# Kernel tuning notes

Hardware: AMD Instinct MI355X
Metric: run time of the kernel (lower is better)

The kernel has to match this reference:

```python
import jax, jax.numpy as jnp
import numpy as np

PARENTS = np.array([0, 0, 1, 2, 3, 0, 5, 6, 7, 0, 9, 10, 11, 12, 11, 14, 15, 16, 11, 18, 19, 20])
SPARSE_JOINTS = [0, 4, 8, 13, 17, 21]
EE = np.array(SPARSE_JOINTS[1:])                       # end effectors (skip root)
NO_SPARSE = np.array([i for i in range(22) if i not in SPARSE_JOINTS])
LAMBDA_EE = 1.0
LAMBDA_EE_REG = 0.1
IDENT_DQ = np.array([1, 0, 0, 0, 0, 0, 0, 0], dtype=np.float32)


def qmul(a, b):
    # Hamilton product, (w, x, y, z) convention
    aw, ax, ay, az = a[..., 0], a[..., 1], a[..., 2], a[..., 3]
    bw, bx, by, bz = b[..., 0], b[..., 1], b[..., 2], b[..., 3]
    return jnp.stack([
        aw * bw - ax * bx - ay * by - az * bz,
        aw * bx + ax * bw + ay * bz - az * by,
        aw * by - ax * bz + ay * bw + az * bx,
        aw * bz + ax * by - ay * bx + az * bw,
    ], axis=-1)


def qconj(q):
    return q * jnp.array([1.0, -1.0, -1.0, -1.0], dtype=q.dtype)


def quat_to_matrix(q, eps=1e-8):
    # normalize then convert to 3x3 rotation matrix
    q = q / jnp.maximum(jnp.linalg.norm(q, axis=-1, keepdims=True), eps)
    w, x, y, z = q[..., 0], q[..., 1], q[..., 2], q[..., 3]
    m = jnp.stack([
        1 - 2 * (y * y + z * z), 2 * (x * y - w * z), 2 * (x * z + w * y),
        2 * (x * y + w * z), 1 - 2 * (x * x + z * z), 2 * (y * z - w * x),
        2 * (x * z - w * y), 2 * (y * z + w * x), 1 - 2 * (x * x + y * y),
    ], axis=-1)
    return m.reshape(q.shape[:-1] + (3, 3))


def denorm_reshape(d, mean, std, set_root):
    # d: (B, 176, T) -> (B, T, 22, 8)
    d = d * std[None, :, None] + mean[None, :, None]
    if set_root:
        d = d.at[:, :8, :].set(jnp.asarray(IDENT_DQ)[None, :, None])
    B, C, T = d.shape
    return d.reshape(B, C // 8, 8, T).transpose(0, 3, 1, 2)


def local_rots(dq):
    # from_root_dual_quat: local_q[j] = conj(global_q[parent[j]]) * global_q[j]
    # (parents always have lower index than children so the original reversed
    # sequential loop reads untouched parent globals -> fully vectorizable)
    qr = dq[..., :4]                       # (B, T, 22, 4) real part
    loc = qmul(qconj(qr[..., PARENTS, :]), qr)
    # root local rotation forced to identity (as in forward_ik)
    return loc.at[..., 0, :].set(jnp.array([1.0, 0.0, 0.0, 0.0], dtype=dq.dtype))


def fk(local_rot, root_pos, offsets):
    # local_rot: (B, T, J, 4); root_pos: (B, T, 3); offsets: (J, 3)
    mats = quat_to_matrix(local_rot)       # (B, T, J, 3, 3)
    gmats = [mats[..., 0, :, :]]
    gpos = [root_pos]
    for j in range(1, PARENTS.shape[0]):   # fixed 22-joint skeleton walk
        p = int(PARENTS[j])
        gmats.append(jnp.matmul(gmats[p], mats[..., j, :, :]))
        gpos.append(jnp.einsum('btij,j->bti', gmats[p], offsets[j]) + gpos[p])
    return jnp.stack(gpos, axis=2), jnp.stack(gmats, axis=2)


def mse(a, b):
    return jnp.mean(jnp.square(a - b))


def setup_inputs() -> dict:
    key = jax.random.key(0)
    ks = jax.random.split(key, 7)
    B, T, J = 32, 4096, 22
    return {
        'input': jax.random.normal(ks[0], (1, 1), dtype=jnp.float32),
        'input_ik': jax.random.normal(ks[1], (B, (J - 1) * 8, T), dtype=jnp.float32),
        'input_decoder': jax.random.normal(ks[2], (B, J * 8, T), dtype=jnp.float32),
        'target': jax.random.normal(ks[3], (B, J * 8, T), dtype=jnp.float32),
        'mean_dqs': jax.random.normal(ks[4], (J * 8,), dtype=jnp.float32) * 0.1,
        'std_dqs': jax.random.uniform(ks[5], (J * 8,), dtype=jnp.float32, minval=0.5, maxval=1.5),
        'offsets': jax.random.normal(ks[6], (J, 3), dtype=jnp.float32),
    }


def reference(input, input_ik, input_decoder, target, mean_dqs, std_dqs, offsets):
    B, _, T = input_ik.shape
    # pad root dq channels with zeros (then overwritten by identity dq)
    dqs = jnp.concatenate([jnp.zeros((B, 8, T), input_ik.dtype), input_ik], axis=1)
    dqs = denorm_reshape(dqs, mean_dqs, std_dqs, set_root=True)            # (B,T,22,8)
    dqs_dec = denorm_reshape(input_decoder, mean_dqs, std_dqs, set_root=True)
    dqs_tgt = denorm_reshape(target, mean_dqs, std_dqs, set_root=False)

    rot_ik = local_rots(dqs)
    rot_dec = local_rots(dqs_dec)
    rot_tgt = local_rots(dqs_tgt)

    root_pos = jnp.zeros((B, T, 3), dtype=input_ik.dtype)
    pos_ik, mat_ik = fk(rot_ik, root_pos, offsets)
    pos_tgt, mat_tgt = fk(rot_tgt, root_pos, offsets)
    pos_dec, mat_dec = fk(rot_dec, root_pos, offsets)

    loss_ee = mse(pos_ik[:, :, EE, :], pos_tgt[:, :, EE, :])
    loss_ee += mse(mat_ik[:, :, EE, :, :], mat_tgt[:, :, EE, :, :])
    loss_reg = mse(pos_dec[:, :, NO_SPARSE, :], pos_ik[:, :, NO_SPARSE, :])
    loss_reg += mse(mat_dec[:, :, NO_SPARSE, :, :], mat_ik[:, :, NO_SPARSE, :, :])
    return loss_ee * LAMBDA_EE + loss_reg * LAMBDA_EE_REG
```

## Files before the change

kernel.cpp:

```cpp
#include <hip/hip_runtime.h>

#define TDIM 4096
#define SBAR() __builtin_amdgcn_sched_barrier(0)

__device__ __forceinline__ void fk_step(float* __restrict__ f,
                                        const float* __restrict__ q,
                                        const float* __restrict__ off) {
  const float pw = f[12], px = f[13], py = f[14], pz = f[15];
  float lw = pw*q[0] + px*q[1] + py*q[2] + pz*q[3];
  float lx = pw*q[1] - px*q[0] - py*q[3] + pz*q[2];
  float ly = pw*q[2] + px*q[3] - py*q[0] - pz*q[1];
  float lz = pw*q[3] - px*q[2] + py*q[1] - pz*q[0];
  float n2 = lw*lw + lx*lx + ly*ly + lz*lz;
  float inv = rsqrtf(fmaxf(n2, 1e-16f));
  lw *= inv; lx *= inv; ly *= inv; lz *= inv;
  float xx = lx*lx, yy = ly*ly, zz = lz*lz;
  float xy = lx*ly, xz = lx*lz, yz = ly*lz;
  float wx = lw*lx, wy = lw*ly, wz = lw*lz;
  float m0 = 1.0f-2.0f*(yy+zz), m1 = 2.0f*(xy-wz),      m2 = 2.0f*(xz+wy);
  float m3 = 2.0f*(xy+wz),      m4 = 1.0f-2.0f*(xx+zz), m5 = 2.0f*(yz-wx);
  float m6 = 2.0f*(xz-wy),      m7 = 2.0f*(yz+wx),      m8 = 1.0f-2.0f*(xx+yy);
  f[9]  += f[0]*off[0] + f[1]*off[1] + f[2]*off[2];
  f[10] += f[3]*off[0] + f[4]*off[1] + f[5]*off[2];
  f[11] += f[6]*off[0] + f[7]*off[1] + f[8]*off[2];
  float r0 = f[0]*m0 + f[1]*m3 + f[2]*m6;
  float r1 = f[0]*m1 + f[1]*m4 + f[2]*m7;
  float r2 = f[0]*m2 + f[1]*m5 + f[2]*m8;
  float r3 = f[3]*m0 + f[4]*m3 + f[5]*m6;
  float r4 = f[3]*m1 + f[4]*m4 + f[5]*m7;
  float r5 = f[3]*m2 + f[4]*m5 + f[5]*m8;
  float r6 = f[6]*m0 + f[7]*m3 + f[8]*m6;
  float r7 = f[6]*m1 + f[7]*m4 + f[8]*m7;
  float r8 = f[6]*m2 + f[7]*m5 + f[8]*m8;
  f[0]=r0; f[1]=r1; f[2]=r2; f[3]=r3; f[4]=r4; f[5]=r5; f[6]=r6; f[7]=r7; f[8]=r8;
  f[12]=q[0]; f[13]=q[1]; f[14]=q[2]; f[15]=q[3];
}

__global__ __launch_bounds__(256) void fk_loss_kernel(
    const float* __restrict__ ik,
    const float* __restrict__ dec,
    const float* __restrict__ tgt,
    const float* __restrict__ mean,
    const float* __restrict__ stdv,
    const float* __restrict__ offs,
    float* __restrict__ out)
{
  __shared__ float s_mean[176];
  __shared__ float s_std[176];
  __shared__ float s_off[66];
  __shared__ float s_wsum[4];
  const int tid = threadIdx.x;
  for (int i = tid; i < 176; i += 256) { s_mean[i] = mean[i]; s_std[i] = stdv[i]; }
  for (int i = tid; i < 66; i += 256) s_off[i] = offs[i];
  __syncthreads();

  const int idx = blockIdx.x * 256 + tid;
  const int b = idx >> 12;
  const int t = idx & 4095;
  const float* __restrict__ pik  = ik  + ((size_t)b * 168) * TDIM + t;
  const float* __restrict__ pdec = dec + ((size_t)b * 176) * TDIM + t;
  const float* __restrict__ ptgt = tgt + ((size_t)b * 176) * TDIM + t;

  float see_p = 0.f, see_m = 0.f, srg_p = 0.f, srg_m = 0.f;

  float fik[16], fdec[16], ftgt[16];
  float sik[16], sdec[16], stgt[16];
  float rq[4];

  float A[23], B[23];

#define LOADST(buf, j)                                                         \
  { _Pragma("unroll")                                                          \
    for (int c = 0; c < 4; c++) buf[c]      = pik [(((j)-1)*8 + c) * TDIM];    \
    _Pragma("unroll")                                                          \
    for (int c = 0; c < 4; c++) buf[4 + c]  = pdec[(((j)*8)   + c) * TDIM];    \
    _Pragma("unroll")                                                          \
    for (int c = 0; c < 4; c++) buf[8 + c]  = ptgt[(((j)*8)   + c) * TDIM];    \
    _Pragma("unroll")                                                          \
    for (int c = 0; c < 4; c++) buf[12 + c] = s_std[(j)*8 + c];                \
    _Pragma("unroll")                                                          \
    for (int c = 0; c < 4; c++) buf[16 + c] = s_mean[(j)*8 + c];               \
    _Pragma("unroll")                                                          \
    for (int c = 0; c < 3; c++) buf[20 + c] = s_off[(j)*3 + c]; }

#define COMP(buf, IS_EE)                                                       \
  { float qi[4], qd[4], qt[4];                                                 \
    _Pragma("unroll")                                                          \
    for (int c = 0; c < 4; c++) {                                              \
      qi[c] = fmaf(buf[c],     buf[12+c], buf[16+c]);                          \
      qd[c] = fmaf(buf[4+c],   buf[12+c], buf[16+c]);                          \
      qt[c] = fmaf(buf[8+c],   buf[12+c], buf[16+c]);                          \
    }                                                                          \
    fk_step(fik,  qi, buf + 20);                                               \
    fk_step(fdec, qd, buf + 20);                                               \
    fk_step(ftgt, qt, buf + 20);                                               \
    if (IS_EE) {                                                               \
      _Pragma("unroll")                                                        \
      for (int c = 0; c < 3; c++) { float d = fik[9+c] - ftgt[9+c]; see_p = fmaf(d, d, see_p); } \
      _Pragma("unroll")                                                        \
      for (int c = 0; c < 9; c++) { float d = fik[c]   - ftgt[c];   see_m = fmaf(d, d, see_m); } \
    } else {                                                                   \
      _Pragma("unroll")                                                        \
      for (int c = 0; c < 3; c++) { float d = fdec[9+c] - fik[9+c]; srg_p = fmaf(d, d, srg_p); } \
      _Pragma("unroll")                                                        \
      for (int c = 0; c < 9; c++) { float d = fdec[c]   - fik[c];   srg_m = fmaf(d, d, srg_m); } \
    } }

#define RESET()                                                                \
  { _Pragma("unroll")                                                          \
    for (int c = 0; c < 16; c++) { fik[c] = 0.f; fdec[c] = 0.f; ftgt[c] = 0.f; } \
    fik[0]=fik[4]=fik[8]=1.f; fdec[0]=fdec[4]=fdec[8]=1.f; ftgt[0]=ftgt[4]=ftgt[8]=1.f; \
    fik[12]=1.f; fdec[12]=1.f;                                                 \
    ftgt[12]=rq[0]; ftgt[13]=rq[1]; ftgt[14]=rq[2]; ftgt[15]=rq[3]; }

#define SAVE()                                                                 \
  { _Pragma("unroll")                                                          \
    for (int c = 0; c < 16; c++) { sik[c]=fik[c]; sdec[c]=fdec[c]; stgt[c]=ftgt[c]; } }

#define RESTORE()                                                              \
  { _Pragma("unroll")                                                          \
    for (int c = 0; c < 16; c++) { fik[c]=sik[c]; fdec[c]=sdec[c]; ftgt[c]=stgt[c]; } }

  float rqr[4], rqs[4], rqm[4];
  #pragma unroll
  for (int c = 0; c < 4; c++) { rqr[c] = ptgt[c * TDIM]; rqs[c] = s_std[c]; rqm[c] = s_mean[c]; }
  LOADST(A, 1);
  SBAR();
  #pragma unroll
  for (int c = 0; c < 4; c++) rq[c] = fmaf(rqr[c], rqs[c], rqm[c]);
  RESET();
  LOADST(B, 2);  COMP(A, false); SBAR();
  LOADST(A, 3);  COMP(B, false); SBAR();
  LOADST(B, 4);  COMP(A, false); SBAR();
  LOADST(A, 5);  COMP(B, true);  RESET(); SBAR();
  LOADST(B, 6);  COMP(A, false); SBAR();
  LOADST(A, 7);  COMP(B, false); SBAR();
  LOADST(B, 8);  COMP(A, false); SBAR();
  LOADST(A, 9);  COMP(B, true);  RESET(); SBAR();
  LOADST(B, 10); COMP(A, false); SBAR();
  LOADST(A, 11); COMP(B, false); SBAR();
  LOADST(B, 12); COMP(A, false); SAVE(); SBAR();
  LOADST(A, 13); COMP(B, false); SBAR();
  LOADST(B, 14); COMP(A, true);  RESTORE(); SBAR();
  LOADST(A, 15); COMP(B, false); SBAR();
  LOADST(B, 16); COMP(A, false); SBAR();
  LOADST(A, 17); COMP(B, false); SBAR();
  LOADST(B, 18); COMP(A, true);  RESTORE(); SBAR();
  LOADST(A, 19); COMP(B, false); SBAR();
  LOADST(B, 20); COMP(A, false); SBAR();
  LOADST(A, 21); COMP(B, false); SBAR();
  COMP(A, true);

#undef LOADST
#undef COMP
#undef RESET
#undef SAVE
#undef RESTORE

  const float W1 = 1.0f / 1966080.0f;
  const float W2 = 1.0f / 5898240.0f;
  const float W3 = 0.1f / 6291456.0f;
  const float W4 = 0.1f / 18874368.0f;
  float val = see_p * W1 + see_m * W2 + srg_p * W3 + srg_m * W4;

  #pragma unroll
  for (int o = 32; o > 0; o >>= 1) val += __shfl_down(val, o, 64);
  const int wid = tid >> 6, lane = tid & 63;
  if (lane == 0) s_wsum[wid] = val;
  __syncthreads();
  if (tid == 0) atomicAdd(out, s_wsum[0] + s_wsum[1] + s_wsum[2] + s_wsum[3]);
}

extern "C" void kernel_launch(void* const* d_in, const int* in_sizes, int n_in,
                              void* d_out, int out_size, void* d_ws, size_t ws_size,
                              hipStream_t stream) {
  const float* ik   = (const float*)d_in[1];
  const float* dec  = (const float*)d_in[2];
  const float* tgt  = (const float*)d_in[3];
  const float* mean = (const float*)d_in[4];
  const float* stdv = (const float*)d_in[5];
  const float* offs = (const float*)d_in[6];
  float* out = (float*)d_out;

  hipMemsetAsync(out, 0, sizeof(float), stream);
  fk_loss_kernel<<<dim3(512), dim3(256), 0, stream>>>(ik, dec, tgt, mean, stdv, offs, out);
}
```

Baseline: 32.84 us.

## Split kinematic chain across two block roles to double parallelism

```diff
diff --git a/kernel.cpp b/kernel.cpp
--- a/kernel.cpp
+++ b/kernel.cpp
@@ -54,7 +54,8 @@
   for (int i = tid; i < 66; i += 256) s_off[i] = offs[i];
   __syncthreads();
 
-  const int idx = blockIdx.x * 256 + tid;
+  const int role = blockIdx.x & 1;
+  const int idx = (blockIdx.x >> 1) * 256 + tid;
   const int b = idx >> 12;
   const int t = idx & 4095;
   const float* __restrict__ pik  = ik  + ((size_t)b * 168) * TDIM + t;
@@ -64,9 +65,7 @@
   float see_p = 0.f, see_m = 0.f, srg_p = 0.f, srg_m = 0.f;
 
   float fik[16], fdec[16], ftgt[16];
-  float sik[16], sdec[16], stgt[16];
   float rq[4];
-
   float A[23], B[23];
 
 #define LOADST(buf, j)                                                         \
@@ -113,49 +112,58 @@
     fik[12]=1.f; fdec[12]=1.f;                                                 \
     ftgt[12]=rq[0]; ftgt[13]=rq[1]; ftgt[14]=rq[2]; ftgt[15]=rq[3]; }
 
-#define SAVE()                                                                 \
-  { _Pragma("unroll")                                                          \
-    for (int c = 0; c < 16; c++) { sik[c]=fik[c]; sdec[c]=fdec[c]; stgt[c]=ftgt[c]; } }
-
-#define RESTORE()                                                              \
-  { _Pragma("unroll")                                                          \
-    for (int c = 0; c < 16; c++) { fik[c]=sik[c]; fdec[c]=sdec[c]; ftgt[c]=stgt[c]; } }
-
   float rqr[4], rqs[4], rqm[4];
   #pragma unroll
   for (int c = 0; c < 4; c++) { rqr[c] = ptgt[c * TDIM]; rqs[c] = s_std[c]; rqm[c] = s_mean[c]; }
-  LOADST(A, 1);
-  SBAR();
-  #pragma unroll
-  for (int c = 0; c < 4; c++) rq[c] = fmaf(rqr[c], rqs[c], rqm[c]);
-  RESET();
-  LOADST(B, 2);  COMP(A, false); SBAR();
-  LOADST(A, 3);  COMP(B, false); SBAR();
-  LOADST(B, 4);  COMP(A, false); SBAR();
-  LOADST(A, 5);  COMP(B, true);  RESET(); SBAR();
-  LOADST(B, 6);  COMP(A, false); SBAR();
-  LOADST(A, 7);  COMP(B, false); SBAR();
-  LOADST(B, 8);  COMP(A, false); SBAR();
-  LOADST(A, 9);  COMP(B, true);  RESET(); SBAR();
-  LOADST(B, 10); COMP(A, false); SBAR();
-  LOADST(A, 11); COMP(B, false); SBAR();
-  LOADST(B, 12); COMP(A, false); SAVE(); SBAR();
-  LOADST(A, 13); COMP(B, false); SBAR();
-  LOADST(B, 14); COMP(A, true);  RESTORE(); SBAR();
-  LOADST(A, 15); COMP(B, false); SBAR();
-  LOADST(B, 16); COMP(A, false); SBAR();
-  LOADST(A, 17); COMP(B, false); SBAR();
-  LOADST(B, 18); COMP(A, true);  RESTORE(); SBAR();
-  LOADST(A, 19); COMP(B, false); SBAR();
-  LOADST(B, 20); COMP(A, false); SBAR();
-  LOADST(A, 21); COMP(B, false); SBAR();
-  COMP(A, true);
+
+  if (role == 0) {
+    LOADST(A, 1);
+    SBAR();
+    #pragma unroll
+    for (int c = 0; c < 4; c++) rq[c] = fmaf(rqr[c], rqs[c], rqm[c]);
+    RESET();
+    LOADST(B, 2);  COMP(A, false); SBAR();
+    LOADST(A, 3);  COMP(B, false); SBAR();
+    LOADST(B, 4);  COMP(A, false); SBAR();
+    LOADST(A, 5);  COMP(B, true);  RESET(); SBAR();
+    LOADST(B, 6);  COMP(A, false); SBAR();
+    LOADST(A, 7);  COMP(B, false); SBAR();
+    LOADST(B, 8);  COMP(A, false); SBAR();
+    COMP(B, true);
+  } else {
+    float sik[16], sdec[16], stgt[16];
+    LOADST(A, 9);
+    SBAR();
+    #pragma unroll
+    for (int c = 0; c < 4; c++) rq[c] = fmaf(rqr[c], rqs[c], rqm[c]);
+    RESET();
+    LOADST(B, 10); COMP(A, false); SBAR();
+    LOADST(A, 11); COMP(B, false); SBAR();
+    LOADST(B, 12); COMP(A, false);
+    #pragma unroll
+    for (int c = 0; c < 16; c++) { sik[c]=fik[c]; sdec[c]=fdec[c]; stgt[c]=ftgt[c]; }
+    SBAR();
+    LOADST(A, 13); COMP(B, false); SBAR();
+    LOADST(B, 14); COMP(A, true);
+    #pragma unroll
+    for (int c = 0; c < 16; c++) { fik[c]=sik[c]; fdec[c]=sdec[c]; ftgt[c]=stgt[c]; }
+    SBAR();
+    LOADST(A, 15); COMP(B, false); SBAR();
+    LOADST(B, 16); COMP(A, false); SBAR();
+    LOADST(A, 17); COMP(B, false); SBAR();
+    LOADST(B, 18); COMP(A, true);
+    #pragma unroll
+    for (int c = 0; c < 16; c++) { fik[c]=sik[c]; fdec[c]=sdec[c]; ftgt[c]=stgt[c]; }
+    SBAR();
+    LOADST(A, 19); COMP(B, false); SBAR();
+    LOADST(B, 20); COMP(A, false); SBAR();
+    LOADST(A, 21); COMP(B, false); SBAR();
+    COMP(A, true);
+  }
 
 #undef LOADST
 #undef COMP
 #undef RESET
-#undef SAVE
-#undef RESTORE
 
   const float W1 = 1.0f / 1966080.0f;
   const float W2 = 1.0f / 5898240.0f;
@@ -183,5 +191,5 @@
   float* out = (float*)d_out;
 
   hipMemsetAsync(out, 0, sizeof(float), stream);
-  fk_loss_kernel<<<dim3(512), dim3(256), 0, stream>>>(ik, dec, tgt, mean, stdv, offs, out);
+  fk_loss_kernel<<<dim3(1024), dim3(256), 0, stream>>>(ik, dec, tgt, mean, stdv, offs, out);
 }
```

After: 123.6 us. 276% more time.

## Cut register pressure: spill FK save state to LDS, load scales lazily

Applied to the files above, without the earlier changes.

```diff
diff --git a/kernel.cpp b/kernel.cpp
--- a/kernel.cpp
+++ b/kernel.cpp
@@ -5,7 +5,7 @@
 
 __device__ __forceinline__ void fk_step(float* __restrict__ f,
                                         const float* __restrict__ q,
-                                        const float* __restrict__ off) {
+                                        float o0, float o1, float o2) {
   const float pw = f[12], px = f[13], py = f[14], pz = f[15];
   float lw = pw*q[0] + px*q[1] + py*q[2] + pz*q[3];
   float lx = pw*q[1] - px*q[0] - py*q[3] + pz*q[2];
@@ -20,9 +20,9 @@
   float m0 = 1.0f-2.0f*(yy+zz), m1 = 2.0f*(xy-wz),      m2 = 2.0f*(xz+wy);
   float m3 = 2.0f*(xy+wz),      m4 = 1.0f-2.0f*(xx+zz), m5 = 2.0f*(yz-wx);
   float m6 = 2.0f*(xz-wy),      m7 = 2.0f*(yz+wx),      m8 = 1.0f-2.0f*(xx+yy);
-  f[9]  += f[0]*off[0] + f[1]*off[1] + f[2]*off[2];
-  f[10] += f[3]*off[0] + f[4]*off[1] + f[5]*off[2];
-  f[11] += f[6]*off[0] + f[7]*off[1] + f[8]*off[2];
+  f[9]  += f[0]*o0 + f[1]*o1 + f[2]*o2;
+  f[10] += f[3]*o0 + f[4]*o1 + f[5]*o2;
+  f[11] += f[6]*o0 + f[7]*o1 + f[8]*o2;
   float r0 = f[0]*m0 + f[1]*m3 + f[2]*m6;
   float r1 = f[0]*m1 + f[1]*m4 + f[2]*m7;
   float r2 = f[0]*m2 + f[1]*m5 + f[2]*m8;
@@ -36,7 +36,7 @@
   f[12]=q[0]; f[13]=q[1]; f[14]=q[2]; f[15]=q[3];
 }
 
-__global__ __launch_bounds__(256) void fk_loss_kernel(
+__global__ __launch_bounds__(256, 4) void fk_loss_kernel(
     const float* __restrict__ ik,
     const float* __restrict__ dec,
     const float* __restrict__ tgt,
@@ -47,11 +47,10 @@
 {
   __shared__ float s_mean[176];
   __shared__ float s_std[176];
-  __shared__ float s_off[66];
+  __shared__ float s_save[36 * 256];
   __shared__ float s_wsum[4];
   const int tid = threadIdx.x;
   for (int i = tid; i < 176; i += 256) { s_mean[i] = mean[i]; s_std[i] = stdv[i]; }
-  for (int i = tid; i < 66; i += 256) s_off[i] = offs[i];
   __syncthreads();
 
   const int idx = blockIdx.x * 256 + tid;
@@ -64,10 +63,9 @@
   float see_p = 0.f, see_m = 0.f, srg_p = 0.f, srg_m = 0.f;
 
   float fik[16], fdec[16], ftgt[16];
-  float sik[16], sdec[16], stgt[16];
   float rq[4];
-
-  float A[23], B[23];
+  float qsv[12];
+  float A[12], B[12];
 
 #define LOADST(buf, j)                                                         \
   { _Pragma("unroll")                                                          \
@@ -75,25 +73,21 @@
     _Pragma("unroll")                                                          \
     for (int c = 0; c < 4; c++) buf[4 + c]  = pdec[(((j)*8)   + c) * TDIM];    \
     _Pragma("unroll")                                                          \
-    for (int c = 0; c < 4; c++) buf[8 + c]  = ptgt[(((j)*8)   + c) * TDIM];    \
-    _Pragma("unroll")                                                          \
-    for (int c = 0; c < 4; c++) buf[12 + c] = s_std[(j)*8 + c];                \
-    _Pragma("unroll")                                                          \
-    for (int c = 0; c < 4; c++) buf[16 + c] = s_mean[(j)*8 + c];               \
-    _Pragma("unroll")                                                          \
-    for (int c = 0; c < 3; c++) buf[20 + c] = s_off[(j)*3 + c]; }
+    for (int c = 0; c < 4; c++) buf[8 + c]  = ptgt[(((j)*8)   + c) * TDIM]; }
 
-#define COMP(buf, IS_EE)                                                       \
+#define COMP(buf, j, IS_EE)                                                    \
   { float qi[4], qd[4], qt[4];                                                 \
     _Pragma("unroll")                                                          \
     for (int c = 0; c < 4; c++) {                                              \
-      qi[c] = fmaf(buf[c],     buf[12+c], buf[16+c]);                          \
-      qd[c] = fmaf(buf[4+c],   buf[12+c], buf[16+c]);                          \
-      qt[c] = fmaf(buf[8+c],   buf[12+c], buf[16+c]);                          \
+      const float sd = s_std[(j)*8 + c], mn = s_mean[(j)*8 + c];               \
+      qi[c] = fmaf(buf[c],     sd, mn);                                        \
+      qd[c] = fmaf(buf[4+c],   sd, mn);                                        \
+      qt[c] = fmaf(buf[8+c],   sd, mn);                                        \
     }                                                                          \
-    fk_step(fik,  qi, buf + 20);                                               \
-    fk_step(fdec, qd, buf + 20);                                               \
-    fk_step(ftgt, qt, buf + 20);                                               \
+    const float o0 = offs[(j)*3], o1 = offs[(j)*3+1], o2 = offs[(j)*3+2];      \
+    fk_step(fik,  qi, o0, o1, o2);                                             \
+    fk_step(fdec, qd, o0, o1, o2);                                             \
+    fk_step(ftgt, qt, o0, o1, o2);                                             \
     if (IS_EE) {                                                               \
       _Pragma("unroll")                                                        \
       for (int c = 0; c < 3; c++) { float d = fik[9+c] - ftgt[9+c]; see_p = fmaf(d, d, see_p); } \
@@ -115,41 +109,53 @@
 
 #define SAVE()                                                                 \
   { _Pragma("unroll")                                                          \
-    for (int c = 0; c < 16; c++) { sik[c]=fik[c]; sdec[c]=fdec[c]; stgt[c]=ftgt[c]; } }
+    for (int c = 0; c < 12; c++) {                                             \
+      s_save[c*256 + tid]      = fik[c];                                       \
+      s_save[(12+c)*256 + tid] = fdec[c];                                      \
+      s_save[(24+c)*256 + tid] = ftgt[c];                                      \
+    }                                                                          \
+    _Pragma("unroll")                                                          \
+    for (int c = 0; c < 4; c++) { qsv[c]=fik[12+c]; qsv[4+c]=fdec[12+c]; qsv[8+c]=ftgt[12+c]; } }
 
 #define RESTORE()                                                              \
   { _Pragma("unroll")                                                          \
-    for (int c = 0; c < 16; c++) { fik[c]=sik[c]; fdec[c]=sdec[c]; ftgt[c]=stgt[c]; } }
+    for (int c = 0; c < 12; c++) {                                             \
+      fik[c]  = s_save[c*256 + tid];                                           \
+      fdec[c] = s_save[(12+c)*256 + tid];                                      \
+      ftgt[c] = s_save[(24+c)*256 + tid];                                      \
+    }                                                                          \
+    _Pragma("unroll")                                                          \
+    for (int c = 0; c < 4; c++) { fik[12+c]=qsv[c]; fdec[12+c]=qsv[4+c]; ftgt[12+c]=qsv[8+c]; } }
 
-  float rqr[4], rqs[4], rqm[4];
+  float rqr[4];
   #pragma unroll
-  for (int c = 0; c < 4; c++) { rqr[c] = ptgt[c * TDIM]; rqs[c] = s_std[c]; rqm[c] = s_mean[c]; }
+  for (int c = 0; c < 4; c++) rqr[c] = ptgt[c * TDIM];
   LOADST(A, 1);
   SBAR();
   #pragma unroll
-  for (int c = 0; c < 4; c++) rq[c] = fmaf(rqr[c], rqs[c], rqm[c]);
+  for (int c = 0; c < 4; c++) rq[c] = fmaf(rqr[c], s_std[c], s_mean[c]);
   RESET();
-  LOADST(B, 2);  COMP(A, false); SBAR();
-  LOADST(A, 3);  COMP(B, false); SBAR();
-  LOADST(B, 4);  COMP(A, false); SBAR();
-  LOADST(A, 5);  COMP(B, true);  RESET(); SBAR();
-  LOADST(B, 6);  COMP(A, false); SBAR();
-  LOADST(A, 7);  COMP(B, false); SBAR();
-  LOADST(B, 8);  COMP(A, false); SBAR();
-  LOADST(A, 9);  COMP(B, true);  RESET(); SBAR();
-  LOADST(B, 10); COMP(A, false); SBAR();
-  LOADST(A, 11); COMP(B, false); SBAR();
-  LOADST(B, 12); COMP(A, false); SAVE(); SBAR();
-  LOADST(A, 13); COMP(B, false); SBAR();
-  LOADST(B, 14); COMP(A, true);  RESTORE(); SBAR();
-  LOADST(A, 15); COMP(B, false); SBAR();
-  LOADST(B, 16); COMP(A, false); SBAR();
-  LOADST(A, 17); COMP(B, false); SBAR();
-  LOADST(B, 18); COMP(A, true);  RESTORE(); SBAR();
-  LOADST(A, 19); COMP(B, false); SBAR();
-  LOADST(B, 20); COMP(A, false); SBAR();
-  LOADST(A, 21); COMP(B, false); SBAR();
-  COMP(A, true);
+  LOADST(B, 2);  COMP(A, 1,  false); SBAR();
+  LOADST(A, 3);  COMP(B, 2,  false); SBAR();
+  LOADST(B, 4);  COMP(A, 3,  false); SBAR();
+  LOADST(A, 5);  COMP(B, 4,  true);  RESET(); SBAR();
+  LOADST(B, 6);  COMP(A, 5,  false); SBAR();
+  LOADST(A, 7);  COMP(B, 6,  false); SBAR();
+  LOADST(B, 8);  COMP(A, 7,  false); SBAR();
+  LOADST(A, 9);  COMP(B, 8,  true);  RESET(); SBAR();
+  LOADST(B, 10); COMP(A, 9,  false); SBAR();
+  LOADST(A, 11); COMP(B, 10, false); SBAR();
+  LOADST(B, 12); COMP(A, 11, false); SAVE(); SBAR();
+  LOADST(A, 13); COMP(B, 12, false); SBAR();
+  LOADST(B, 14); COMP(A, 13, true);  RESTORE(); SBAR();
+  LOADST(A, 15); COMP(B, 14, false); SBAR();
+  LOADST(B, 16); COMP(A, 15, false); SBAR();
+  LOADST(A, 17); COMP(B, 16, false); SBAR();
+  LOADST(B, 18); COMP(A, 17, true);  RESTORE(); SBAR();
+  LOADST(A, 19); COMP(B, 18, false); SBAR();
+  LOADST(B, 20); COMP(A, 19, false); SBAR();
+  LOADST(A, 21); COMP(B, 20, false); SBAR();
+  COMP(A, 21, true);
 
 #undef LOADST
 #undef COMP
```

After: 35.38 us. 7.7% more time.
